# Performance work log

Hardware: AMD Instinct MI355X
Metric: run time of the kernel (lower is better)

## Reference

```python
import jax, jax.numpy as jnp
import numpy as np

# e2m1 FP4 lookup table (MXFP4)
FP4_VALUES = jnp.array([0.0, 0.5, 1.0, 1.5, 2.0, 3.0, 4.0, 6.0,
                        -0.0, -0.5, -1.0, -1.5, -2.0, -3.0, -4.0, -6.0], dtype=jnp.float32)
BLOCK = 32  # MXFP4/MXFP8 block size
SWIGLU_LIMIT = 7.0
SWIGLU_ALPHA = 1.702


def mxfp8_qdq(x):
    """Quantize-dequantize x to MXFP8: fp8_e4m3 mantissas with per-32-block E8M0 scales."""
    shp = x.shape
    nb = shp[-1] // BLOCK
    xb = x.reshape(*shp[:-1], nb, BLOCK)
    max_abs = jnp.max(jnp.abs(xb), axis=-1, keepdims=True)
    e = jnp.clip(jnp.ceil(jnp.log2(jnp.maximum(max_abs, 1e-12))), -127.0, 128.0)
    scale = jnp.exp2(e)
    xq = (xb / scale).astype(jnp.float8_e4m3fn).astype(x.dtype) * scale
    return xq.reshape(shp)


def dequant_mxfp4(blocks, scales):
    """blocks: [..., g, 16] int (packed nibbles), scales: [..., g] int (E8M0 biased 127).
    Returns [..., g*32] float32, low nibble first within each byte."""
    lo = FP4_VALUES[blocks & 15]
    hi = FP4_VALUES[blocks >> 4]
    vals = jnp.stack([lo, hi], axis=-1).reshape(*blocks.shape[:-1], BLOCK)  # interleave lo,hi
    e = (scales - 127).astype(jnp.float32)
    w = vals * jnp.exp2(e)[..., None]
    return w.reshape(*blocks.shape[:-2], blocks.shape[-2] * BLOCK)


def moe_forward(hidden_states, expert_indices, routing_weights,
                gate_up_blocks, gate_up_scales, gate_up_bias,
                down_blocks, down_scales, down_bias):
    w_gu = dequant_mxfp4(gate_up_blocks, gate_up_scales)  # [E, 2I, H]
    w_d = dequant_mxfp4(down_blocks, down_scales)          # [E, H, I]
    xq = mxfp8_qdq(hidden_states)                          # [T, H] mxfp8 qdq (row-blockwise)

    def one_expert(wgu, bgu, wd, bd):
        h = xq @ wgu.T + bgu                               # [T, 2I]
        gate = jnp.minimum(h[..., 0::2], SWIGLU_LIMIT)     # interleaved gate/up
        up = jnp.clip(h[..., 1::2], -SWIGLU_LIMIT, SWIGLU_LIMIT)
        glu = gate * jax.nn.sigmoid(SWIGLU_ALPHA * gate)
        act = (up + 1.0) * glu                             # [T, I]
        return mxfp8_qdq(act) @ wd.T + bd                  # [T, H]

    expert_outs = jax.vmap(one_expert)(w_gu, gate_up_bias, w_d, down_bias)  # [E, T, H]
    T = hidden_states.shape[0]
    sel = expert_outs[expert_indices, jnp.arange(T)[:, None]]  # [T, K, H]
    return jnp.sum(routing_weights[..., None] * sel, axis=1)   # [T, H]


def setup_inputs() -> dict:
    key = jax.random.key(0)
    ks = jax.random.split(key, 9)
    E, T, K, H, I = 8, 1024, 2, 2880, 2880
    return {
        'hidden_states': jax.random.normal(ks[0], (T, H), dtype=jnp.float32),
        'expert_indices': jax.random.randint(ks[1], (T, K), 0, E, dtype=jnp.int32),
        'routing_weights': jax.random.uniform(ks[2], (T, K), dtype=jnp.float32),
        'gate_up_blocks': jax.random.randint(ks[3], (E, 2 * I, H // 32, 16), 0, 256, dtype=jnp.int32),
        'gate_up_scales': jax.random.randint(ks[4], (E, 2 * I, H // 32), 0, 132, dtype=jnp.int32),
        'gate_up_bias': jax.random.normal(ks[5], (E, 2 * I), dtype=jnp.float32),
        'down_blocks': jax.random.randint(ks[6], (E, H, I // 32, 16), 0, 256, dtype=jnp.int32),
        'down_scales': jax.random.randint(ks[7], (E, H, I // 32), 0, 132, dtype=jnp.int32),
        'down_bias': jax.random.normal(ks[8], (E, H), dtype=jnp.float32),
    }


def reference(hidden_states, expert_indices, routing_weights,
              gate_up_blocks, gate_up_scales, gate_up_bias,
              down_blocks, down_scales, down_bias):
    return moe_forward(hidden_states, expert_indices, routing_weights,
                       gate_up_blocks, gate_up_scales, gate_up_bias,
                       down_blocks, down_scales, down_bias)
```

## Files before the change

### kernel.cpp

```cpp
#include <hip/hip_runtime.h>
#include <math.h>

#define T_TOK 1024
#define E_EXP 8
#define H_DIM 2880
#define I_DIM 2880
#define NGU   5760
#define KB    90
#define TM 128
#define TN 128
#define MAXROWS 3072

typedef __attribute__((ext_vector_type(8))) short short8;
typedef __attribute__((ext_vector_type(4))) float f32x4;

#define PERM(a, b, s) __builtin_amdgcn_perm((uint)(a), (uint)(b), (uint)(s))

#define XQ_OFF   0ull
#define ACT_OFF  5898240ull
#define RTOK_OFF 23592960ull
#define RW_OFF   23605248ull
#define EB_OFF   23617536ull
#define EPC_OFF  23617568ull
#define CGU_OFF  23617664ull
#define CGS_OFF  89972864ull
#define CDB_OFF  94120064ull
#define CDS_OFF  127297664ull
#define WS_NEED  129371264ull

__device__ inline ushort f2bf(float f) {
  unsigned u = __float_as_uint(f);
  unsigned r = u + 0x7FFFu + ((u >> 16) & 1u);
  return (ushort)(r >> 16);
}

__device__ inline int blk_exp(float amax) {
  amax = fmaxf(amax, 1e-12f);
  unsigned b = __float_as_uint(amax);
  int e = (int)(b >> 23) - 127;
  if (b & 0x7FFFFFu) e += 1;
  return min(max(e, -127), 128);
}

__device__ inline float qdq_val(float v, int eblk) {
  float av = fabsf(v);
  if (av == 0.f) return 0.f;
  int fl = (int)(__float_as_uint(av) >> 23) - 127 - eblk;
  int p = max(fl, -6) - 3;
  float step = ldexpf(1.f, p + eblk);
  return rintf(v / step) * step;
}

__device__ inline float fp4v(int n) {
  int mag = n & 7;
  float v;
  if (mag == 0) v = 0.f;
  else if (mag == 1) v = 0.5f;
  else v = ldexpf(1.0f + 0.5f * (float)(mag & 1), (mag >> 1) - 1);
  return (n & 8) ? -v : v;
}

__device__ inline uint dec_byte(const float2* lut, int b, float sc) {
  float2 l = lut[b & 255];
  uint lo = __float_as_uint(l.x * sc);
  uint hi = __float_as_uint(l.y * sc);
  return PERM(hi, lo, 0x07060302u);
}

struct BTbl { uint tlo_l, tlo_h, thi_l, thi_h; };

__device__ inline BTbl build_tbl(float sc) {
  uint g0 = 0u;
  uint g1 = __float_as_uint(0.5f * sc);
  uint g2 = __float_as_uint(sc);
  uint g3 = __float_as_uint(1.5f * sc);
  uint g4 = __float_as_uint(2.0f * sc);
  uint g5 = __float_as_uint(3.0f * sc);
  uint g6 = __float_as_uint(4.0f * sc);
  uint g7 = __float_as_uint(6.0f * sc);
  uint p01 = PERM(g1, g0, 0x07030602u);
  uint p23 = PERM(g3, g2, 0x07030602u);
  uint p45 = PERM(g5, g4, 0x07030602u);
  uint p67 = PERM(g7, g6, 0x07030602u);
  BTbl t;
  t.tlo_l = PERM(p23, p01, 0x05040100u);
  t.thi_l = PERM(p23, p01, 0x07060302u);
  t.tlo_h = PERM(p67, p45, 0x05040100u);
  t.thi_h = PERM(p67, p45, 0x07060302u);
  return t;
}

__device__ inline uint4 dec_w(uint w, const BTbl& t) {
  uint ml = w & 0x07070707u;
  uint mh = (w >> 4) & 0x07070707u;
  uint sl = (w << 4) & 0x80808080u;
  uint sh = w & 0x80808080u;
  uint hl = PERM(t.thi_h, t.thi_l, ml) | sl;
  uint hh = PERM(t.thi_h, t.thi_l, mh) | sh;
  uint ll = PERM(t.tlo_h, t.tlo_l, ml);
  uint lh = PERM(t.tlo_h, t.tlo_l, mh);
  uint4 o;
  o.x = PERM(hl, ll, 0x05010400u);
  o.y = PERM(hl, ll, 0x07030602u);
  o.z = PERM(hh, lh, 0x05010400u);
  o.w = PERM(hh, lh, 0x07030602u);
  return o;
}

__device__ inline uint4 aperm(uint4 u) {
  uint4 v;
  v.x = PERM(u.y, u.x, 0x05040100u);
  v.y = PERM(u.w, u.z, 0x05040100u);
  v.z = PERM(u.y, u.x, 0x07060302u);
  v.w = PERM(u.w, u.z, 0x07060302u);
  return v;
}

__global__ void repack_kernel(const int* __restrict__ src, uint4* __restrict__ dst, int n16) {
  int g = blockIdx.x * 256 + threadIdx.x;
  if (g >= n16) return;
  const int4* s = (const int4*)(src) + g * 4;
  int4 w0 = s[0], w1 = s[1], w2 = s[2], w3 = s[3];
  uint4 o;
  o.x = (uint)(w0.x & 255) | ((uint)(w0.y & 255) << 8) | ((uint)(w0.z & 255) << 16) | ((uint)(w0.w) << 24);
  o.y = (uint)(w1.x & 255) | ((uint)(w1.y & 255) << 8) | ((uint)(w1.z & 255) << 16) | ((uint)(w1.w) << 24);
  o.z = (uint)(w2.x & 255) | ((uint)(w2.y & 255) << 8) | ((uint)(w2.z & 255) << 16) | ((uint)(w2.w) << 24);
  o.w = (uint)(w3.x & 255) | ((uint)(w3.y & 255) << 8) | ((uint)(w3.z & 255) << 16) | ((uint)(w3.w) << 24);
  dst[g] = o;
}

__global__ void quant_x_kernel(const float* __restrict__ x, ushort* __restrict__ xq) {
  int g = blockIdx.x * 256 + threadIdx.x;
  float4 v4 = ((const float4*)x)[g];
  float am = fmaxf(fmaxf(fabsf(v4.x), fabsf(v4.y)), fmaxf(fabsf(v4.z), fabsf(v4.w)));
  am = fmaxf(am, __shfl_xor(am, 1));
  am = fmaxf(am, __shfl_xor(am, 2));
  am = fmaxf(am, __shfl_xor(am, 4));
  int eb = blk_exp(am);
  ushort4 o;
  o.x = f2bf(qdq_val(v4.x, eb));
  o.y = f2bf(qdq_val(v4.y, eb));
  o.z = f2bf(qdq_val(v4.z, eb));
  o.w = f2bf(qdq_val(v4.w, eb));
  ((ushort4*)xq)[g] = o;
}

__global__ void routing_kernel(const int* __restrict__ eidx, const float* __restrict__ rwt,
                               int* __restrict__ rtok, float* __restrict__ rw,
                               int* __restrict__ ebase, int* __restrict__ epc) {
  __shared__ int cnt[E_EXP];
  __shared__ int base_s[E_EXP];
  __shared__ int pos[E_EXP];
  int t = threadIdx.x;
  if (t < E_EXP) cnt[t] = 0;
  __syncthreads();
  for (int p = t; p < T_TOK * 2; p += 256) atomicAdd(&cnt[eidx[p]], 1);
  __syncthreads();
  if (t == 0) {
    int b = 0;
    for (int e = 0; e < E_EXP; e++) {
      base_s[e] = b;
      b += ((cnt[e] + TM - 1) / TM) * TM;
    }
  }
  __syncthreads();
  if (t < E_EXP) {
    pos[t] = 0;
    ebase[t] = base_s[t];
    epc[t] = ((cnt[t] + TM - 1) / TM) * TM;
  }
  __syncthreads();
  for (int p = t; p < T_TOK * 2; p += 256) {
    int e = eidx[p];
    int o = atomicAdd(&pos[e], 1);
    rtok[base_s[e] + o] = p >> 1;
    rw[base_s[e] + o] = rwt[p];
  }
  __syncthreads();
  for (int e = 0; e < E_EXP; e++) {
    int c = cnt[e], pc = ((c + TM - 1) / TM) * TM;
    for (int i = c + t; i < pc; i += 256) {
      rtok[base_s[e] + i] = 0;
      rw[base_s[e] + i] = 0.f;
    }
  }
}

__global__ __launch_bounds__(256, 2)
void gemm1c_kernel(const ushort* __restrict__ xq,
                   const uchar* __restrict__ cgu, const uchar* __restrict__ cgs,
                   const float* __restrict__ gubias,
                   const int* __restrict__ rtok, const int* __restrict__ ebase,
                   const int* __restrict__ epc,
                   ushort* __restrict__ act) {
  const int ntile = blockIdx.x;
  const int e = blockIdx.y >> 4;
  const int mtile = blockIdx.y & 15;
  if (mtile * TM >= epc[e]) return;
  const int rowbase = ebase[e] + mtile * TM;

  __shared__ __align__(16) ushort lA[TM][40];
  __shared__ __align__(16) ushort lB[TN][40];

  const int tid = threadIdx.x;
  const int wave = tid >> 6, lane = tid & 63;
  const int half = tid & 1, srow = tid >> 1;
  const int wm = (wave & 1) * 64, wn = (wave >> 1) * 64;
  const int lrow = lane & 15, q = lane >> 4;

  const int tokA = rtok[rowbase + srow];
  const ushort* aSrc = xq + tokA * H_DIM + half * 16;
  const int nrow = ntile * TN + srow;
  const uchar* bSrc = cgu + (size_t)(e * NGU + nrow) * 1440 + half * 8;
  const uchar* sSrc = cgs + (size_t)(e * NGU + nrow) * KB;

  f32x4 acc[4][4];
#pragma unroll
  for (int i = 0; i < 4; i++)
#pragma unroll
    for (int j = 0; j < 4; j++) acc[i][j] = (f32x4){0.f, 0.f, 0.f, 0.f};

  uint4 a0 = ((const uint4*)(aSrc))[0];
  uint4 a1 = ((const uint4*)(aSrc))[1];
  uint2 bw = *(const uint2*)(bSrc);
  uchar sb = sSrc[0];

  for (int kb = 0; kb < KB; kb++) {
    const int nk = (kb + 1 < KB) ? kb + 1 : kb;
    uint4 na0 = ((const uint4*)(aSrc + nk * 32))[0];
    uint4 na1 = ((const uint4*)(aSrc + nk * 32))[1];
    uint2 nbw = *(const uint2*)(bSrc + nk * 16);
    uchar nsb = sSrc[nk];

    float sc = ldexpf(1.f, (int)sb - 127);
    BTbl t = build_tbl(sc);
    uint4 d0 = dec_w(bw.x, t);
    uint4 d1 = dec_w(bw.y, t);
    uint4 pa0 = aperm(a0);
    uint4 pa1 = aperm(a1);

    __syncthreads();
    *(uint4*)&lA[srow][half * 16] = pa0;
    *(uint4*)&lA[srow][half * 16 + 8] = pa1;
    *(uint4*)&lB[srow][half * 16] = d0;
    *(uint4*)&lB[srow][half * 16 + 8] = d1;
    __syncthreads();

    short8 af[4], bfr[4];
#pragma unroll
    for (int mi = 0; mi < 4; mi++) af[mi] = *(const short8*)&lA[wm + mi * 16 + lrow][q * 8];
#pragma unroll
    for (int ni = 0; ni < 4; ni++) bfr[ni] = *(const short8*)&lB[wn + ni * 16 + lrow][q * 8];
#pragma unroll
    for (int mi = 0; mi < 4; mi++)
#pragma unroll
      for (int ni = 0; ni < 4; ni++)
        acc[mi][ni] = __builtin_amdgcn_mfma_f32_16x16x32_bf16(af[mi], bfr[ni], acc[mi][ni], 0, 0, 0);

    a0 = na0; a1 = na1; bw = nbw; sb = nsb;
  }

  const int nbase = ntile * TN + wn;
  float bias_v[4];
#pragma unroll
  for (int ni = 0; ni < 4; ni++) bias_v[ni] = gubias[e * NGU + nbase + ni * 16 + lrow];
  const bool evenl = (lane & 1) == 0;
#pragma unroll
  for (int mi = 0; mi < 4; mi++) {
    float av[4][4];
#pragma unroll
    for (int ni = 0; ni < 4; ni++)
#pragma unroll
      for (int r = 0; r < 4; r++) {
        float h = acc[mi][ni][r] + bias_v[ni];
        float pp = __shfl_xor(h, 1);
        float gate = evenl ? h : pp;
        float up = evenl ? pp : h;
        gate = fminf(gate, 7.f);
        up = fminf(fmaxf(up, -7.f), 7.f);
        float glu = gate / (1.f + expf(-1.702f * gate));
        av[ni][r] = (up + 1.f) * glu;
      }
#pragma unroll
    for (int r = 0; r < 4; r++) {
      float am = 0.f;
#pragma unroll
      for (int ni = 0; ni < 4; ni++) am = fmaxf(am, fabsf(av[ni][r]));
      am = fmaxf(am, __shfl_xor(am, 2));
      am = fmaxf(am, __shfl_xor(am, 4));
      am = fmaxf(am, __shfl_xor(am, 8));
      int eb = blk_exp(am);
      if (evenl) {
        int row = rowbase + wm + mi * 16 + q * 4 + r;
        int cb = (nbase >> 1) + (lrow >> 1);
#pragma unroll
        for (int ni = 0; ni < 4; ni++)
          act[row * I_DIM + cb + ni * 8] = f2bf(qdq_val(av[ni][r], eb));
      }
    }
  }
}

__global__ __launch_bounds__(256, 2)
void gemm2c_kernel(const ushort* __restrict__ act,
                   const uchar* __restrict__ cdb, const uchar* __restrict__ cds,
                   const float* __restrict__ dbias,
                   const int* __restrict__ rtok, const float* __restrict__ rw,
                   const int* __restrict__ ebase, const int* __restrict__ epc,
                   float* __restrict__ out) {
  const int ntile = blockIdx.x;
  const int e = blockIdx.y >> 4;
  const int mtile = blockIdx.y & 15;
  if (mtile * TM >= epc[e]) return;
  const int rowbase = ebase[e] + mtile * TM;
  const int kz = blockIdx.z;
  const int kb0 = kz * (KB / 2), kb1 = kb0 + (KB / 2);

  __shared__ __align__(16) ushort lA[TM][40];
  __shared__ __align__(16) ushort lB[TN][40];

  const int tid = threadIdx.x;
  const int wave = tid >> 6, lane = tid & 63;
  const int half = tid & 1, srow = tid >> 1;
  const int wm = (wave & 1) * 64, wn = (wave >> 1) * 64;
  const int lrow = lane & 15, q = lane >> 4;

  const ushort* aSrc = act + (size_t)(rowbase + srow) * I_DIM + half * 16;
  int nrow = ntile * TN + srow;
  if (nrow >= H_DIM) nrow = H_DIM - 1;
  const uchar* bSrc = cdb + (size_t)(e * H_DIM + nrow) * 1440 + half * 8;
  const uchar* sSrc = cds + (size_t)(e * H_DIM + nrow) * KB;

  f32x4 acc[4][4];
#pragma unroll
  for (int i = 0; i < 4; i++)
#pragma unroll
    for (int j = 0; j < 4; j++) acc[i][j] = (f32x4){0.f, 0.f, 0.f, 0.f};

  uint4 a0 = ((const uint4*)(aSrc + kb0 * 32))[0];
  uint4 a1 = ((const uint4*)(aSrc + kb0 * 32))[1];
  uint2 bw = *(const uint2*)(bSrc + kb0 * 16);
  uchar sb = sSrc[kb0];

  for (int kb = kb0; kb < kb1; kb++) {
    const int nk = (kb + 1 < kb1) ? kb + 1 : kb;
    uint4 na0 = ((const uint4*)(aSrc + nk * 32))[0];
    uint4 na1 = ((const uint4*)(aSrc + nk * 32))[1];
    uint2 nbw = *(const uint2*)(bSrc + nk * 16);
    uchar nsb = sSrc[nk];

    float sc = ldexpf(1.f, (int)sb - 127);
    BTbl t = build_tbl(sc);
    uint4 d0 = dec_w(bw.x, t);
    uint4 d1 = dec_w(bw.y, t);
    uint4 pa0 = aperm(a0);
    uint4 pa1 = aperm(a1);

    __syncthreads();
    *(uint4*)&lA[srow][half * 16] = pa0;
    *(uint4*)&lA[srow][half * 16 + 8] = pa1;
    *(uint4*)&lB[srow][half * 16] = d0;
    *(uint4*)&lB[srow][half * 16 + 8] = d1;
    __syncthreads();

    short8 af[4], bfr[4];
#pragma unroll
    for (int mi = 0; mi < 4; mi++) af[mi] = *(const short8*)&lA[wm + mi * 16 + lrow][q * 8];
#pragma unroll
    for (int ni = 0; ni < 4; ni++) bfr[ni] = *(const short8*)&lB[wn + ni * 16 + lrow][q * 8];
#pragma unroll
    for (int mi = 0; mi < 4; mi++)
#pragma unroll
      for (int ni = 0; ni < 4; ni++)
        acc[mi][ni] = __builtin_amdgcn_mfma_f32_16x16x32_bf16(af[mi], bfr[ni], acc[mi][ni], 0, 0, 0);

    a0 = na0; a1 = na1; bw = nbw; sb = nsb;
  }

  const int nbase = ntile * TN + wn;
  float bias_v[4];
#pragma unroll
  for (int ni = 0; ni < 4; ni++) {
    int n = nbase + ni * 16 + lrow;
    bias_v[ni] = (kz == 0 && n < H_DIM) ? dbias[e * H_DIM + n] : 0.f;
  }
#pragma unroll
  for (int mi = 0; mi < 4; mi++)
#pragma unroll
    for (int r = 0; r < 4; r++) {
      int orow = rowbase + wm + mi * 16 + q * 4 + r;
      int tok = rtok[orow];
      float w = rw[orow];
      if (w != 0.f) {
#pragma unroll
        for (int ni = 0; ni < 4; ni++) {
          int n = nbase + ni * 16 + lrow;
          if (n < H_DIM) atomicAdd(&out[tok * H_DIM + n], w * (acc[mi][ni][r] + bias_v[ni]));
        }
      }
    }
}

__global__ __launch_bounds__(256, 2)
void gemm1_kernel(const ushort* __restrict__ xq,
                  const int* __restrict__ gub, const int* __restrict__ gus,
                  const float* __restrict__ gubias,
                  const int* __restrict__ rtok, const int* __restrict__ ebase,
                  const int* __restrict__ epc,
                  ushort* __restrict__ act) {
  const int ntile = blockIdx.x;
  const int e = blockIdx.y >> 4;
  const int mtile = blockIdx.y & 15;
  if (mtile * TM >= epc[e]) return;
  const int rowbase = ebase[e] + mtile * TM;

  __shared__ __align__(16) ushort lA[TM][40];
  __shared__ __align__(16) ushort lB[TN][40];
  __shared__ float2 lut[256];

  const int tid = threadIdx.x;
  lut[tid] = make_float2(fp4v(tid & 15), fp4v((tid >> 4) & 15));
  __syncthreads();

  const int wave = tid >> 6, lane = tid & 63;
  const int half = tid & 1, srow = tid >> 1;
  const int wm = (wave & 1) * 64, wn = (wave >> 1) * 64;
  const int lrow = lane & 15, q = lane >> 4;

  const int tokA = rtok[rowbase + srow];
  const ushort* aSrc = xq + tokA * H_DIM + half * 16;
  const int nrow = ntile * TN + srow;
  const int* bSrc = gub + ((e * NGU + nrow) * KB) * 16 + half * 8;
  const int* sSrc = gus + (e * NGU + nrow) * KB;

  f32x4 acc[4][4];
#pragma unroll
  for (int i = 0; i < 4; i++)
#pragma unroll
    for (int j = 0; j < 4; j++) acc[i][j] = (f32x4){0.f, 0.f, 0.f, 0.f};

  for (int kb = 0; kb < KB; kb++) {
    uint4 a0 = ((const uint4*)(aSrc + kb * 32))[0];
    uint4 a1 = ((const uint4*)(aSrc + kb * 32))[1];
    int4 b0 = ((const int4*)(bSrc + kb * 16))[0];
    int4 b1 = ((const int4*)(bSrc + kb * 16))[1];
    float sc = ldexpf(1.f, sSrc[kb] - 127);
    int bv[8] = {b0.x, b0.y, b0.z, b0.w, b1.x, b1.y, b1.z, b1.w};
    uint us[8];
#pragma unroll
    for (int j = 0; j < 8; j++) us[j] = dec_byte(lut, bv[j], sc);
    __syncthreads();
    *(uint4*)&lA[srow][half * 16] = a0;
    *(uint4*)&lA[srow][half * 16 + 8] = a1;
    uint4 w0; w0.x = us[0]; w0.y = us[1]; w0.z = us[2]; w0.w = us[3];
    uint4 w1; w1.x = us[4]; w1.y = us[5]; w1.z = us[6]; w1.w = us[7];
    *(uint4*)&lB[srow][half * 16] = w0;
    *(uint4*)&lB[srow][half * 16 + 8] = w1;
    __syncthreads();
    short8 af[4], bfr[4];
#pragma unroll
    for (int mi = 0; mi < 4; mi++) af[mi] = *(const short8*)&lA[wm + mi * 16 + lrow][q * 8];
#pragma unroll
    for (int ni = 0; ni < 4; ni++) bfr[ni] = *(const short8*)&lB[wn + ni * 16 + lrow][q * 8];
#pragma unroll
    for (int mi = 0; mi < 4; mi++)
#pragma unroll
      for (int ni = 0; ni < 4; ni++)
        acc[mi][ni] = __builtin_amdgcn_mfma_f32_16x16x32_bf16(af[mi], bfr[ni], acc[mi][ni], 0, 0, 0);
  }

  const int nbase = ntile * TN + wn;
  float bias_v[4];
#pragma unroll
  for (int ni = 0; ni < 4; ni++) bias_v[ni] = gubias[e * NGU + nbase + ni * 16 + lrow];
  const bool evenl = (lane & 1) == 0;
#pragma unroll
  for (int mi = 0; mi < 4; mi++) {
    float av[4][4];
#pragma unroll
    for (int ni = 0; ni < 4; ni++)
#pragma unroll
      for (int r = 0; r < 4; r++) {
        float h = acc[mi][ni][r] + bias_v[ni];
        float pp = __shfl_xor(h, 1);
        float gate = evenl ? h : pp;
        float up = evenl ? pp : h;
        gate = fminf(gate, 7.f);
        up = fminf(fmaxf(up, -7.f), 7.f);
        float glu = gate / (1.f + expf(-1.702f * gate));
        av[ni][r] = (up + 1.f) * glu;
      }
#pragma unroll
    for (int r = 0; r < 4; r++) {
      float am = 0.f;
#pragma unroll
      for (int ni = 0; ni < 4; ni++) am = fmaxf(am, fabsf(av[ni][r]));
      am = fmaxf(am, __shfl_xor(am, 2));
      am = fmaxf(am, __shfl_xor(am, 4));
      am = fmaxf(am, __shfl_xor(am, 8));
      int eb = blk_exp(am);
      if (evenl) {
        int row = rowbase + wm + mi * 16 + q * 4 + r;
        int cb = (nbase >> 1) + (lrow >> 1);
#pragma unroll
        for (int ni = 0; ni < 4; ni++)
          act[row * I_DIM + cb + ni * 8] = f2bf(qdq_val(av[ni][r], eb));
      }
    }
  }
}

__global__ __launch_bounds__(256, 2)
void gemm2_kernel(const ushort* __restrict__ act,
                  const int* __restrict__ db, const int* __restrict__ dsc,
                  const float* __restrict__ dbias,
                  const int* __restrict__ rtok, const float* __restrict__ rw,
                  const int* __restrict__ ebase, const int* __restrict__ epc,
                  float* __restrict__ out) {
  const int ntile = blockIdx.x;
  const int e = blockIdx.y >> 4;
  const int mtile = blockIdx.y & 15;
  if (mtile * TM >= epc[e]) return;
  const int rowbase = ebase[e] + mtile * TM;
  const int kz = blockIdx.z;
  const int kb0 = kz * (KB / 2), kb1 = kb0 + (KB / 2);

  __shared__ __align__(16) ushort lA[TM][40];
  __shared__ __align__(16) ushort lB[TN][40];
  __shared__ float2 lut[256];

  const int tid = threadIdx.x;
  lut[tid] = make_float2(fp4v(tid & 15), fp4v((tid >> 4) & 15));
  __syncthreads();

  const int wave = tid >> 6, lane = tid & 63;
  const int half = tid & 1, srow = tid >> 1;
  const int wm = (wave & 1) * 64, wn = (wave >> 1) * 64;
  const int lrow = lane & 15, q = lane >> 4;

  const ushort* aSrc = act + (rowbase + srow) * I_DIM + half * 16;
  int nrow = ntile * TN + srow;
  if (nrow >= H_DIM) nrow = H_DIM - 1;
  const int* bSrc = db + ((e * H_DIM + nrow) * KB) * 16 + half * 8;
  const int* sSrc = dsc + (e * H_DIM + nrow) * KB;

  f32x4 acc[4][4];
#pragma unroll
  for (int i = 0; i < 4; i++)
#pragma unroll
    for (int j = 0; j < 4; j++) acc[i][j] = (f32x4){0.f, 0.f, 0.f, 0.f};

  for (int kb = kb0; kb < kb1; kb++) {
    uint4 a0 = ((const uint4*)(aSrc + kb * 32))[0];
    uint4 a1 = ((const uint4*)(aSrc + kb * 32))[1];
    int4 b0 = ((const int4*)(bSrc + kb * 16))[0];
    int4 b1 = ((const int4*)(bSrc + kb * 16))[1];
    float sc = ldexpf(1.f, sSrc[kb] - 127);
    int bv[8] = {b0.x, b0.y, b0.z, b0.w, b1.x, b1.y, b1.z, b1.w};
    uint us[8];
#pragma unroll
    for (int j = 0; j < 8; j++) us[j] = dec_byte(lut, bv[j], sc);
    __syncthreads();
    *(uint4*)&lA[srow][half * 16] = a0;
    *(uint4*)&lA[srow][half * 16 + 8] = a1;
    uint4 w0; w0.x = us[0]; w0.y = us[1]; w0.z = us[2]; w0.w = us[3];
    uint4 w1; w1.x = us[4]; w1.y = us[5]; w1.z = us[6]; w1.w = us[7];
    *(uint4*)&lB[srow][half * 16] = w0;
    *(uint4*)&lB[srow][half * 16 + 8] = w1;
    __syncthreads();
    short8 af[4], bfr[4];
#pragma unroll
    for (int mi = 0; mi < 4; mi++) af[mi] = *(const short8*)&lA[wm + mi * 16 + lrow][q * 8];
#pragma unroll
    for (int ni = 0; ni < 4; ni++) bfr[ni] = *(const short8*)&lB[wn + ni * 16 + lrow][q * 8];
#pragma unroll
    for (int mi = 0; mi < 4; mi++)
#pragma unroll
      for (int ni = 0; ni < 4; ni++)
        acc[mi][ni] = __builtin_amdgcn_mfma_f32_16x16x32_bf16(af[mi], bfr[ni], acc[mi][ni], 0, 0, 0);
  }

  const int nbase = ntile * TN + wn;
  float bias_v[4];
#pragma unroll
  for (int ni = 0; ni < 4; ni++) {
    int n = nbase + ni * 16 + lrow;
    bias_v[ni] = (kz == 0 && n < H_DIM) ? dbias[e * H_DIM + n] : 0.f;
  }
#pragma unroll
  for (int mi = 0; mi < 4; mi++)
#pragma unroll
    for (int r = 0; r < 4; r++) {
      int orow = rowbase + wm + mi * 16 + q * 4 + r;
      int tok = rtok[orow];
      float w = rw[orow];
      if (w != 0.f) {
#pragma unroll
        for (int ni = 0; ni < 4; ni++) {
          int n = nbase + ni * 16 + lrow;
          if (n < H_DIM) atomicAdd(&out[tok * H_DIM + n], w * (acc[mi][ni][r] + bias_v[ni]));
        }
      }
    }
}

extern "C" void kernel_launch(void* const* d_in, const int* in_sizes, int n_in,
                              void* d_out, int out_size, void* d_ws, size_t ws_size,
                              hipStream_t stream) {
  const float* hs = (const float*)d_in[0];
  const int* eidx = (const int*)d_in[1];
  const float* rwt = (const float*)d_in[2];
  const int* gub = (const int*)d_in[3];
  const int* gus = (const int*)d_in[4];
  const float* gubias = (const float*)d_in[5];
  const int* db = (const int*)d_in[6];
  const int* dsc = (const int*)d_in[7];
  const float* dbias = (const float*)d_in[8];
  float* out = (float*)d_out;
  char* ws = (char*)d_ws;

  ushort* xq = (ushort*)(ws + XQ_OFF);
  ushort* act = (ushort*)(ws + ACT_OFF);
  int* rtok = (int*)(ws + RTOK_OFF);
  float* rw = (float*)(ws + RW_OFF);
  int* ebase = (int*)(ws + EB_OFF);
  int* epc = (int*)(ws + EPC_OFF);

  hipMemsetAsync(d_out, 0, (size_t)out_size * sizeof(float), stream);
  quant_x_kernel<<<2880, 256, 0, stream>>>(hs, xq);
  routing_kernel<<<1, 256, 0, stream>>>(eidx, rwt, rtok, rw, ebase, epc);

  if (ws_size >= WS_NEED) {
    uchar* cgu = (uchar*)(ws + CGU_OFF);
    uchar* cgs = (uchar*)(ws + CGS_OFF);
    uchar* cdb = (uchar*)(ws + CDB_OFF);
    uchar* cds = (uchar*)(ws + CDS_OFF);
    repack_kernel<<<16200, 256, 0, stream>>>(gub, (uint4*)cgu, 4147200);
    repack_kernel<<<8100, 256, 0, stream>>>(db, (uint4*)cdb, 2073600);
    repack_kernel<<<1013, 256, 0, stream>>>(gus, (uint4*)cgs, 259200);
    repack_kernel<<<507, 256, 0, stream>>>(dsc, (uint4*)cds, 129600);
    gemm1c_kernel<<<dim3(45, 128), 256, 0, stream>>>(xq, cgu, cgs, gubias, rtok, ebase, epc, act);
    gemm2c_kernel<<<dim3(23, 128, 2), 256, 0, stream>>>(act, cdb, cds, dbias, rtok, rw, ebase, epc, out);
  } else {
    gemm1_kernel<<<dim3(45, 128), 256, 0, stream>>>(xq, gub, gus, gubias, rtok, ebase, epc, act);
    gemm2_kernel<<<dim3(23, 128, 2), 256, 0, stream>>>(act, db, dsc, dbias, rtok, rw, ebase, epc, out);
  }
}
```

Measured before the change: 816.6 us.

## Use native MXFP8xMXFP4 scaled MFMA with runtime layout probe and bf16 fallback

Adds a probe kernel that runs the scaled f8f6f4 MFMA on synthetic data at runtime to find the correct nibble order and scale-lane mapping. When the probe succeeds, new GEMM kernels feed fp8 activations and raw packed fp4 weights straight into mfma_scale 32x32x64, with per-block E8M0 scales staged in LDS. This removes the in-loop fp4-to-bf16 dequantization and halves the activation bytes. Activations are quantized to fp8 bytes in the epilogue, and scales are repacked into k-major arrays. The bf16 kernels remain as a flag-gated fallback, which adds extra launches that exit early, and the B operand pads half its register lanes with zeros.

```diff
diff --git a/kernel.cpp b/kernel.cpp
--- a/kernel.cpp
+++ b/kernel.cpp
@@ -12,21 +12,28 @@
 #define MAXROWS 3072
 
 typedef __attribute__((ext_vector_type(8))) short short8;
+typedef __attribute__((ext_vector_type(8))) int i32x8;
 typedef __attribute__((ext_vector_type(4))) float f32x4;
+typedef __attribute__((ext_vector_type(16))) float f32x16;
 
 #define PERM(a, b, s) __builtin_amdgcn_perm((uint)(a), (uint)(b), (uint)(s))
 
-#define XQ_OFF   0ull
-#define ACT_OFF  5898240ull
-#define RTOK_OFF 23592960ull
-#define RW_OFF   23605248ull
-#define EB_OFF   23617536ull
-#define EPC_OFF  23617568ull
-#define CGU_OFF  23617664ull
-#define CGS_OFF  89972864ull
-#define CDB_OFF  94120064ull
-#define CDS_OFF  127297664ull
-#define WS_NEED  129371264ull
+#define FLAGS_OFF 0ull
+#define EB_OFF    16ull
+#define EPC_OFF   48ull
+#define RTOK_OFF  128ull
+#define RW_OFF    12416ull
+#define CGU_OFF   24704ull
+#define CDB_OFF   66379904ull
+#define WGS_OFF   99557504ull
+#define WDS_OFF   103704704ull
+#define PATH_OFF  105778304ull
+#define XQ_OFF    (PATH_OFF)
+#define ACT_OFF   (PATH_OFF + 5898240ull)
+#define XQ8_OFF   (PATH_OFF)
+#define XS8_OFF   (PATH_OFF + 2949120ull)
+#define ACT8_OFF  (PATH_OFF + 3041280ull)
+#define AS8_OFF   (PATH_OFF + 11888640ull)
 
 __device__ inline ushort f2bf(float f) {
   unsigned u = __float_as_uint(f);
@@ -51,6 +58,17 @@
   return rintf(v / step) * step;
 }
 
+__device__ inline uint fp8_byte_exact(float x) {
+  uint u = __float_as_uint(x);
+  uint s = (u >> 24) & 0x80u;
+  float ax = fabsf(x);
+  if (ax == 0.f) return s;
+  int E = (int)((u >> 23) & 0xFFu) - 127;
+  uint M = (u >> 20) & 7u;
+  if (E >= -6) return s | (uint)((E + 7) << 3) | M;
+  return s | (uint)(int)(ax * 512.f + 0.5f);
+}
+
 __device__ inline float fp4v(int n) {
   int mag = n & 7;
   float v;
@@ -60,11 +78,8 @@
   return (n & 8) ? -v : v;
 }
 
-__device__ inline uint dec_byte(const float2* lut, int b, float sc) {
-  float2 l = lut[b & 255];
-  uint lo = __float_as_uint(l.x * sc);
-  uint hi = __float_as_uint(l.y * sc);
-  return PERM(hi, lo, 0x07060302u);
+__device__ inline uint nibswap(uint w) {
+  return ((w & 0x0F0F0F0Fu) << 4) | ((w >> 4) & 0x0F0F0F0Fu);
 }
 
 struct BTbl { uint tlo_l, tlo_h, thi_l, thi_h; };
@@ -116,20 +131,77 @@
   return v;
 }
 
-__global__ void repack_kernel(const int* __restrict__ src, uint4* __restrict__ dst, int n16) {
-  int g = blockIdx.x * 256 + threadIdx.x;
-  if (g >= n16) return;
-  const int4* s = (const int4*)(src) + g * 4;
-  int4 w0 = s[0], w1 = s[1], w2 = s[2], w3 = s[3];
-  uint4 o;
-  o.x = (uint)(w0.x & 255) | ((uint)(w0.y & 255) << 8) | ((uint)(w0.z & 255) << 16) | ((uint)(w0.w) << 24);
-  o.y = (uint)(w1.x & 255) | ((uint)(w1.y & 255) << 8) | ((uint)(w1.z & 255) << 16) | ((uint)(w1.w) << 24);
-  o.z = (uint)(w2.x & 255) | ((uint)(w2.y & 255) << 8) | ((uint)(w2.z & 255) << 16) | ((uint)(w2.w) << 24);
-  o.w = (uint)(w3.x & 255) | ((uint)(w3.y & 255) << 8) | ((uint)(w3.z & 255) << 16) | ((uint)(w3.w) << 24);
-  dst[g] = o;
-}
-
-__global__ void quant_x_kernel(const float* __restrict__ x, ushort* __restrict__ xq) {
+__global__ void probe_kernel(int* __restrict__ flags) {
+  const int l = threadIdx.x;
+  const int l31 = l & 31, h = l >> 5;
+  const uint E4[7] = {0x00u, 0x38u, 0x40u, 0x44u, 0x48u, 0x4Au, 0x4Cu};
+
+  i32x8 af;
+#pragma unroll
+  for (int r8 = 0; r8 < 8; r8++) {
+    uint w = 0;
+#pragma unroll
+    for (int b = 0; b < 4; b++) {
+      int k = h * 32 + r8 * 4 + b;
+      int v = ((l31 + 3 * k) % 13) - 6;
+      uint byte = E4[v < 0 ? -v : v] | (v < 0 ? 0x80u : 0u);
+      w |= byte << (8 * b);
+    }
+    af[r8] = (int)w;
+  }
+  i32x8 b0v, b1v;
+#pragma unroll
+  for (int i = 0; i < 8; i++) { b0v[i] = 0; b1v[i] = 0; }
+#pragma unroll
+  for (int r4 = 0; r4 < 4; r4++) {
+    uint w0 = 0, w1 = 0;
+#pragma unroll
+    for (int i = 0; i < 4; i++) {
+      int k0 = h * 32 + r4 * 8 + 2 * i;
+      uint c0 = (uint)((k0 * 5 + l31 * 3) & 15);
+      uint c1 = (uint)(((k0 + 1) * 5 + l31 * 3) & 15);
+      w0 |= (c0 | (c1 << 4)) << (8 * i);
+      w1 |= (c1 | (c0 << 4)) << (8 * i);
+    }
+    b0v[r4] = (int)w0;
+    b1v[r4] = (int)w1;
+  }
+
+  f32x16 z;
+#pragma unroll
+  for (int i = 0; i < 16; i++) z[i] = 0.f;
+
+  int best = -1, mask = 0;
+  for (int c = 0; c < 4; c++) {
+    int f1 = c & 1, f2 = (c >> 1) & 1;
+    i32x8 bb = f1 ? b1v : b0v;
+    int kidx = h ^ f2;
+    int sa = 127 + ((l31 + kidx) & 3);
+    int sb = 127 - ((l31 + kidx) & 1);
+    f32x16 d = __builtin_amdgcn_mfma_scale_f32_32x32x64_f8f6f4(af, bb, z, 0, 4, 0, sa, 0, sb);
+    bool ok = true;
+#pragma unroll
+    for (int r = 0; r < 16; r++) {
+      int row = (r & 3) + 8 * (r >> 2) + 4 * h;
+      float ref = 0.f;
+      for (int k = 0; k < 64; k++) {
+        float fa = (float)(((row + 3 * k) % 13) - 6) * exp2f((float)((row + (k >> 5)) & 3));
+        float fb = fp4v((k * 5 + l31 * 3) & 15) * exp2f(-(float)((l31 + (k >> 5)) & 1));
+        ref += fa * fb;
+      }
+      if (fabsf(d[r] - ref) > 0.25f) ok = false;
+    }
+    if (__all((int)ok)) {
+      mask |= (1 << c);
+      if (best < 0) best = c;
+    }
+  }
+  if (l == 0) { flags[0] = best; flags[1] = mask; }
+}
+
+__global__ void quant_x_kernel(const int* __restrict__ flags,
+                               const float* __restrict__ x, ushort* __restrict__ xq) {
+  if (flags[0] >= 0) return;
   int g = blockIdx.x * 256 + threadIdx.x;
   float4 v4 = ((const float4*)x)[g];
   float am = fmaxf(fmaxf(fabsf(v4.x), fabsf(v4.y)), fmaxf(fabsf(v4.z), fabsf(v4.w)));
@@ -143,6 +215,30 @@
   o.z = f2bf(qdq_val(v4.z, eb));
   o.w = f2bf(qdq_val(v4.w, eb));
   ((ushort4*)xq)[g] = o;
+}
+
+__global__ void quant_x8_kernel(const int* __restrict__ flags,
+                                const float* __restrict__ x, uint* __restrict__ xq8,
+                                uchar* __restrict__ xs8) {
+  if (flags[0] < 0) return;
+  int g = blockIdx.x * 256 + threadIdx.x;
+  float4 v = ((const float4*)x)[g];
+  float am = fmaxf(fmaxf(fabsf(v.x), fabsf(v.y)), fmaxf(fabsf(v.z), fabsf(v.w)));
+  am = fmaxf(am, __shfl_xor(am, 1));
+  am = fmaxf(am, __shfl_xor(am, 2));
+  am = fmaxf(am, __shfl_xor(am, 4));
+  int eb = blk_exp(am);
+  float s = ldexpf(1.f, -eb);
+  uint b0 = fp8_byte_exact(qdq_val(v.x * s, 0));
+  uint b1 = fp8_byte_exact(qdq_val(v.y * s, 0));
+  uint b2 = fp8_byte_exact(qdq_val(v.z * s, 0));
+  uint b3 = fp8_byte_exact(qdq_val(v.w * s, 0));
+  xq8[g] = b0 | (b1 << 8) | (b2 << 16) | (b3 << 24);
+  if ((g & 7) == 0) {
+    int tok = g / 720;
+    int kb = (g - tok * 720) >> 3;
+    xs8[kb * T_TOK + tok] = (uchar)(eb + 127);
+  }
 }
 
 __global__ void routing_kernel(const int* __restrict__ eidx, const float* __restrict__ rwt,
@@ -186,19 +282,287 @@
   }
 }
 
-__global__ __launch_bounds__(256, 2)
-void gemm1c_kernel(const ushort* __restrict__ xq,
-                   const uchar* __restrict__ cgu, const uchar* __restrict__ cgs,
+__global__ void repack_kernel(const int* __restrict__ flags,
+                              const int* __restrict__ src, uint4* __restrict__ dst, int n16) {
+  int g = blockIdx.x * 256 + threadIdx.x;
+  if (g >= n16) return;
+  uint f1 = (flags[0] >= 0 && (flags[0] & 1)) ? 1u : 0u;
+  const int4* s = (const int4*)(src) + g * 4;
+  int4 w0 = s[0], w1 = s[1], w2 = s[2], w3 = s[3];
+  uint4 o;
+  o.x = (uint)(w0.x & 255) | ((uint)(w0.y & 255) << 8) | ((uint)(w0.z & 255) << 16) | ((uint)(w0.w) << 24);
+  o.y = (uint)(w1.x & 255) | ((uint)(w1.y & 255) << 8) | ((uint)(w1.z & 255) << 16) | ((uint)(w1.w) << 24);
+  o.z = (uint)(w2.x & 255) | ((uint)(w2.y & 255) << 8) | ((uint)(w2.z & 255) << 16) | ((uint)(w2.w) << 24);
+  o.w = (uint)(w3.x & 255) | ((uint)(w3.y & 255) << 8) | ((uint)(w3.z & 255) << 16) | ((uint)(w3.w) << 24);
+  if (f1) { o.x = nibswap(o.x); o.y = nibswap(o.y); o.z = nibswap(o.z); o.w = nibswap(o.w); }
+  dst[g] = o;
+}
+
+__global__ void repack_scale_kernel(const int* __restrict__ src, uchar* __restrict__ dst, int R) {
+  int r = blockIdx.x * 256 + threadIdx.x;
+  int kb = blockIdx.y;
+  dst[(size_t)kb * R + r] = (uchar)src[(size_t)r * KB + kb];
+}
+
+__global__ __launch_bounds__(256, 3)
+void gemm1s_kernel(const int* __restrict__ flags,
+                   const uchar* __restrict__ xq8, const uchar* __restrict__ xs8,
+                   const uchar* __restrict__ cgu, const uchar* __restrict__ wgs,
                    const float* __restrict__ gubias,
                    const int* __restrict__ rtok, const int* __restrict__ ebase,
                    const int* __restrict__ epc,
-                   ushort* __restrict__ act) {
+                   uchar* __restrict__ act8, uchar* __restrict__ as8) {
+  const int fl = flags[0];
+  if (fl < 0) return;
+  const int f2 = (fl >> 1) & 1;
   const int ntile = blockIdx.x;
   const int e = blockIdx.y >> 4;
   const int mtile = blockIdx.y & 15;
   if (mtile * TM >= epc[e]) return;
   const int rowbase = ebase[e] + mtile * TM;
 
+  __shared__ __align__(16) uchar lA[128 * 80];
+  __shared__ __align__(16) uchar lB[128 * 48];
+  __shared__ uchar sAs[KB * 128];
+  __shared__ uchar sBs[KB * 128];
+  __shared__ int ltok[128];
+
+  const int tid = threadIdx.x;
+  const int wave = tid >> 6, lane = tid & 63;
+  const int half = tid & 1, srow = tid >> 1;
+  const int wm = (wave & 1) * 64, wn = (wave >> 1) * 64;
+  const int l31 = lane & 31, l5 = lane >> 5;
+
+  if (tid < 128) ltok[tid] = rtok[rowbase + tid];
+  __syncthreads();
+  for (int i = tid; i < KB * 128; i += 256) {
+    int kb = i >> 7, r = i & 127;
+    sAs[i] = xs8[kb * T_TOK + ltok[r]];
+    sBs[i] = wgs[(size_t)kb * 46080 + e * NGU + ntile * 128 + r];
+  }
+
+  const int tokA = ltok[srow];
+  const uchar* aSrc = xq8 + (size_t)tokA * H_DIM + half * 32;
+  const int nrow = ntile * TN + srow;
+  const uchar* bSrc = cgu + (size_t)(e * NGU + nrow) * 1440 + half * 16;
+
+  f32x16 acc[2][2];
+#pragma unroll
+  for (int i = 0; i < 2; i++)
+#pragma unroll
+    for (int j = 0; j < 2; j++)
+#pragma unroll
+      for (int r = 0; r < 16; r++) acc[i][j][r] = 0.f;
+
+  uint4 pa0 = *(const uint4*)(aSrc);
+  uint4 pa1 = *(const uint4*)(aSrc + 16);
+  uint4 pb = *(const uint4*)(bSrc);
+
+  for (int kb2 = 0; kb2 < 45; kb2++) {
+    const int nk = (kb2 + 1 < 45) ? kb2 + 1 : kb2;
+    uint4 na0 = *(const uint4*)(aSrc + nk * 64);
+    uint4 na1 = *(const uint4*)(aSrc + nk * 64 + 16);
+    uint4 nb = *(const uint4*)(bSrc + nk * 32);
+
+    __syncthreads();
+    *(uint4*)&lA[srow * 80 + half * 32] = pa0;
+    *(uint4*)&lA[srow * 80 + half * 32 + 16] = pa1;
+    *(uint4*)&lB[srow * 48 + half * 16] = pb;
+    __syncthreads();
+
+    i32x8 af[2], bf2[2];
+    int sa[2], sb[2];
+#pragma unroll
+    for (int f = 0; f < 2; f++) {
+      const uchar* pr = &lA[(wm + f * 32 + l31) * 80 + l5 * 32];
+      uint4 lo = *(const uint4*)pr;
+      uint4 hi = *(const uint4*)(pr + 16);
+      af[f][0] = lo.x; af[f][1] = lo.y; af[f][2] = lo.z; af[f][3] = lo.w;
+      af[f][4] = hi.x; af[f][5] = hi.y; af[f][6] = hi.z; af[f][7] = hi.w;
+      uint4 bb = *(const uint4*)&lB[(wn + f * 32 + l31) * 48 + l5 * 16];
+      bf2[f][0] = bb.x; bf2[f][1] = bb.y; bf2[f][2] = bb.z; bf2[f][3] = bb.w;
+      bf2[f][4] = 0; bf2[f][5] = 0; bf2[f][6] = 0; bf2[f][7] = 0;
+      int kidx = kb2 * 2 + (l5 ^ f2);
+      sa[f] = sAs[kidx * 128 + wm + f * 32 + l31];
+      sb[f] = sBs[kidx * 128 + wn + f * 32 + l31];
+    }
+#pragma unroll
+    for (int fm = 0; fm < 2; fm++)
+#pragma unroll
+      for (int fn = 0; fn < 2; fn++)
+        acc[fm][fn] = __builtin_amdgcn_mfma_scale_f32_32x32x64_f8f6f4(
+            af[fm], bf2[fn], acc[fm][fn], 0, 4, 0, sa[fm], 0, sb[fn]);
+
+    pa0 = na0; pa1 = na1; pb = nb;
+  }
+
+  const int nb0 = ntile * 128 + wn;
+  const float bias0 = gubias[e * NGU + nb0 + l31];
+  const float bias1 = gubias[e * NGU + nb0 + 32 + l31];
+  const bool evenl = (lane & 1) == 0;
+  const int cb_ix = ntile * 2 + (wn >> 6);
+  const int cbase = ntile * 64 + (wn >> 1) + (l31 >> 1);
+#pragma unroll
+  for (int fm = 0; fm < 2; fm++) {
+#pragma unroll
+    for (int r = 0; r < 16; r++) {
+      int row = rowbase + wm + fm * 32 + (r & 3) + 8 * (r >> 2) + l5 * 4;
+      float h0 = acc[fm][0][r] + bias0;
+      float h1 = acc[fm][1][r] + bias1;
+      float p0 = __shfl_xor(h0, 1);
+      float p1 = __shfl_xor(h1, 1);
+      float g0 = evenl ? h0 : p0, u0 = evenl ? p0 : h0;
+      float g1 = evenl ? h1 : p1, u1 = evenl ? p1 : h1;
+      g0 = fminf(g0, 7.f); u0 = fminf(fmaxf(u0, -7.f), 7.f);
+      g1 = fminf(g1, 7.f); u1 = fminf(fmaxf(u1, -7.f), 7.f);
+      float a0 = (u0 + 1.f) * (g0 / (1.f + expf(-1.702f * g0)));
+      float a1 = (u1 + 1.f) * (g1 / (1.f + expf(-1.702f * g1)));
+      float am = fmaxf(fabsf(a0), fabsf(a1));
+      am = fmaxf(am, __shfl_xor(am, 2));
+      am = fmaxf(am, __shfl_xor(am, 4));
+      am = fmaxf(am, __shfl_xor(am, 8));
+      am = fmaxf(am, __shfl_xor(am, 16));
+      int eb = blk_exp(am);
+      if (l31 == 0) as8[(size_t)cb_ix * MAXROWS + row] = (uchar)(eb + 127);
+      if (evenl) {
+        float s = ldexpf(1.f, -eb);
+        act8[(size_t)row * I_DIM + cbase] = (uchar)fp8_byte_exact(qdq_val(a0 * s, 0));
+        act8[(size_t)row * I_DIM + cbase + 16] = (uchar)fp8_byte_exact(qdq_val(a1 * s, 0));
+      }
+    }
+  }
+}
+
+__global__ __launch_bounds__(256, 3)
+void gemm2s_kernel(const int* __restrict__ flags,
+                   const uchar* __restrict__ act8, const uchar* __restrict__ as8,
+                   const uchar* __restrict__ cdb, const uchar* __restrict__ wds,
+                   const float* __restrict__ dbias,
+                   const int* __restrict__ rtok, const float* __restrict__ rw,
+                   const int* __restrict__ ebase, const int* __restrict__ epc,
+                   float* __restrict__ out) {
+  const int fl = flags[0];
+  if (fl < 0) return;
+  const int f2 = (fl >> 1) & 1;
+  const int ntile = blockIdx.x;
+  const int e = blockIdx.y >> 4;
+  const int mtile = blockIdx.y & 15;
+  if (mtile * TM >= epc[e]) return;
+  const int rowbase = ebase[e] + mtile * TM;
+  const int kz = blockIdx.z;
+  const int klo = kz * 23;
+  const int khi = kz ? 45 : 23;
+
+  __shared__ __align__(16) uchar lA[128 * 80];
+  __shared__ __align__(16) uchar lB[128 * 48];
+  __shared__ uchar sAs[KB * 128];
+  __shared__ uchar sBs[KB * 128];
+
+  const int tid = threadIdx.x;
+  const int wave = tid >> 6, lane = tid & 63;
+  const int half = tid & 1, srow = tid >> 1;
+  const int wm = (wave & 1) * 64, wn = (wave >> 1) * 64;
+  const int l31 = lane & 31, l5 = lane >> 5;
+
+  for (int i = tid; i < KB * 128; i += 256) {
+    int kb = i >> 7, r = i & 127;
+    int rr = min(ntile * 128 + r, H_DIM - 1);
+    sAs[i] = as8[(size_t)kb * MAXROWS + rowbase + r];
+    sBs[i] = wds[(size_t)kb * 23040 + e * H_DIM + rr];
+  }
+
+  const uchar* aSrc = act8 + (size_t)(rowbase + srow) * I_DIM + half * 32;
+  const int nrow = min(ntile * TN + srow, H_DIM - 1);
+  const uchar* bSrc = cdb + (size_t)(e * H_DIM + nrow) * 1440 + half * 16;
+
+  f32x16 acc[2][2];
+#pragma unroll
+  for (int i = 0; i < 2; i++)
+#pragma unroll
+    for (int j = 0; j < 2; j++)
+#pragma unroll
+      for (int r = 0; r < 16; r++) acc[i][j][r] = 0.f;
+
+  uint4 pa0 = *(const uint4*)(aSrc + klo * 64);
+  uint4 pa1 = *(const uint4*)(aSrc + klo * 64 + 16);
+  uint4 pb = *(const uint4*)(bSrc + klo * 32);
+
+  for (int kb2 = klo; kb2 < khi; kb2++) {
+    const int nk = (kb2 + 1 < khi) ? kb2 + 1 : kb2;
+    uint4 na0 = *(const uint4*)(aSrc + nk * 64);
+    uint4 na1 = *(const uint4*)(aSrc + nk * 64 + 16);
+    uint4 nb = *(const uint4*)(bSrc + nk * 32);
+
+    __syncthreads();
+    *(uint4*)&lA[srow * 80 + half * 32] = pa0;
+    *(uint4*)&lA[srow * 80 + half * 32 + 16] = pa1;
+    *(uint4*)&lB[srow * 48 + half * 16] = pb;
+    __syncthreads();
+
+    i32x8 af[2], bf2[2];
+    int sa[2], sb[2];
+#pragma unroll
+    for (int f = 0; f < 2; f++) {
+      const uchar* pr = &lA[(wm + f * 32 + l31) * 80 + l5 * 32];
+      uint4 lo = *(const uint4*)pr;
+      uint4 hi = *(const uint4*)(pr + 16);
+      af[f][0] = lo.x; af[f][1] = lo.y; af[f][2] = lo.z; af[f][3] = lo.w;
+      af[f][4] = hi.x; af[f][5] = hi.y; af[f][6] = hi.z; af[f][7] = hi.w;
+      uint4 bb = *(const uint4*)&lB[(wn + f * 32 + l31) * 48 + l5 * 16];
+      bf2[f][0] = bb.x; bf2[f][1] = bb.y; bf2[f][2] = bb.z; bf2[f][3] = bb.w;
+      bf2[f][4] = 0; bf2[f][5] = 0; bf2[f][6] = 0; bf2[f][7] = 0;
+      int kidx = kb2 * 2 + (l5 ^ f2);
+      sa[f] = sAs[kidx * 128 + wm + f * 32 + l31];
+      sb[f] = sBs[kidx * 128 + wn + f * 32 + l31];
+    }
+#pragma unroll
+    for (int fm = 0; fm < 2; fm++)
+#pragma unroll
+      for (int fn = 0; fn < 2; fn++)
+        acc[fm][fn] = __builtin_amdgcn_mfma_scale_f32_32x32x64_f8f6f4(
+            af[fm], bf2[fn], acc[fm][fn], 0, 4, 0, sa[fm], 0, sb[fn]);
+
+    pa0 = na0; pa1 = na1; pb = nb;
+  }
+
+  const int nb0 = ntile * 128 + wn;
+  float bias0 = 0.f, bias1 = 0.f;
+  if (kz == 0) {
+    bias0 = (nb0 + l31 < H_DIM) ? dbias[e * H_DIM + nb0 + l31] : 0.f;
+    bias1 = (nb0 + 32 + l31 < H_DIM) ? dbias[e * H_DIM + nb0 + 32 + l31] : 0.f;
+  }
+#pragma unroll
+  for (int fm = 0; fm < 2; fm++) {
+#pragma unroll
+    for (int r = 0; r < 16; r++) {
+      int orow = rowbase + wm + fm * 32 + (r & 3) + 8 * (r >> 2) + l5 * 4;
+      int tok = rtok[orow];
+      float w = rw[orow];
+      if (w != 0.f) {
+        int n0 = nb0 + l31;
+        int n1 = nb0 + 32 + l31;
+        if (n0 < H_DIM) atomicAdd(&out[(size_t)tok * H_DIM + n0], w * (acc[fm][0][r] + bias0));
+        if (n1 < H_DIM) atomicAdd(&out[(size_t)tok * H_DIM + n1], w * (acc[fm][1][r] + bias1));
+      }
+    }
+  }
+}
+
+__global__ __launch_bounds__(256, 2)
+void gemm1c_kernel(const int* __restrict__ flags,
+                   const ushort* __restrict__ xq,
+                   const uchar* __restrict__ cgu, const uchar* __restrict__ wgs,
+                   const float* __restrict__ gubias,
+                   const int* __restrict__ rtok, const int* __restrict__ ebase,
+                   const int* __restrict__ epc,
+                   ushort* __restrict__ act) {
+  if (flags[0] >= 0) return;
+  const int ntile = blockIdx.x;
+  const int e = blockIdx.y >> 4;
+  const int mtile = blockIdx.y & 15;
+  if (mtile * TM >= epc[e]) return;
+  const int rowbase = ebase[e] + mtile * TM;
+
   __shared__ __align__(16) ushort lA[TM][40];
   __shared__ __align__(16) ushort lB[TN][40];
 
@@ -212,7 +576,7 @@
   const ushort* aSrc = xq + tokA * H_DIM + half * 16;
   const int nrow = ntile * TN + srow;
   const uchar* bSrc = cgu + (size_t)(e * NGU + nrow) * 1440 + half * 8;
-  const uchar* sSrc = cgs + (size_t)(e * NGU + nrow) * KB;
+  const uchar* sSrc = wgs + (size_t)(e * NGU + nrow);
 
   f32x4 acc[4][4];
 #pragma unroll
@@ -230,7 +594,7 @@
     uint4 na0 = ((const uint4*)(aSrc + nk * 32))[0];
     uint4 na1 = ((const uint4*)(aSrc + nk * 32))[1];
     uint2 nbw = *(const uint2*)(bSrc + nk * 16);
-    uchar nsb = sSrc[nk];
+    uchar nsb = sSrc[(size_t)nk * 46080];
 
     float sc = ldexpf(1.f, (int)sb - 127);
     BTbl t = build_tbl(sc);
@@ -302,12 +666,14 @@
 }
 
 __global__ __launch_bounds__(256, 2)
-void gemm2c_kernel(const ushort* __restrict__ act,
-                   const uchar* __restrict__ cdb, const uchar* __restrict__ cds,
+void gemm2c_kernel(const int* __restrict__ flags,
+                   const ushort* __restrict__ act,
+                   const uchar* __restrict__ cdb, const uchar* __restrict__ wds,
                    const float* __restrict__ dbias,
                    const int* __restrict__ rtok, const float* __restrict__ rw,
                    const int* __restrict__ ebase, const int* __restrict__ epc,
                    float* __restrict__ out) {
+  if (flags[0] >= 0) return;
   const int ntile = blockIdx.x;
   const int e = blockIdx.y >> 4;
   const int mtile = blockIdx.y & 15;
@@ -329,7 +695,7 @@
   int nrow = ntile * TN + srow;
   if (nrow >= H_DIM) nrow = H_DIM - 1;
   const uchar* bSrc = cdb + (size_t)(e * H_DIM + nrow) * 1440 + half * 8;
-  const uchar* sSrc = cds + (size_t)(e * H_DIM + nrow) * KB;
+  const uchar* sSrc = wds + (size_t)(e * H_DIM + nrow);
 
   f32x4 acc[4][4];
 #pragma unroll
@@ -340,14 +706,14 @@
   uint4 a0 = ((const uint4*)(aSrc + kb0 * 32))[0];
   uint4 a1 = ((const uint4*)(aSrc + kb0 * 32))[1];
   uint2 bw = *(const uint2*)(bSrc + kb0 * 16);
-  uchar sb = sSrc[kb0];
+  uchar sb = sSrc[(size_t)kb0 * 23040];
 
   for (int kb = kb0; kb < kb1; kb++) {
     const int nk = (kb + 1 < kb1) ? kb + 1 : kb;
     uint4 na0 = ((const uint4*)(aSrc + nk * 32))[0];
     uint4 na1 = ((const uint4*)(aSrc + nk * 32))[1];
     uint2 nbw = *(const uint2*)(bSrc + nk * 16);
-    uchar nsb = sSrc[nk];
+    uchar nsb = sSrc[(size_t)nk * 23040];
 
     float sc = ldexpf(1.f, (int)sb - 127);
     BTbl t = build_tbl(sc);
@@ -375,209 +741,6 @@
         acc[mi][ni] = __builtin_amdgcn_mfma_f32_16x16x32_bf16(af[mi], bfr[ni], acc[mi][ni], 0, 0, 0);
 
     a0 = na0; a1 = na1; bw = nbw; sb = nsb;
-  }
-
-  const int nbase = ntile * TN + wn;
-  float bias_v[4];
-#pragma unroll
-  for (int ni = 0; ni < 4; ni++) {
-    int n = nbase + ni * 16 + lrow;
-    bias_v[ni] = (kz == 0 && n < H_DIM) ? dbias[e * H_DIM + n] : 0.f;
-  }
-#pragma unroll
-  for (int mi = 0; mi < 4; mi++)
-#pragma unroll
-    for (int r = 0; r < 4; r++) {
-      int orow = rowbase + wm + mi * 16 + q * 4 + r;
-      int tok = rtok[orow];
-      float w = rw[orow];
-      if (w != 0.f) {
-#pragma unroll
-        for (int ni = 0; ni < 4; ni++) {
-          int n = nbase + ni * 16 + lrow;
-          if (n < H_DIM) atomicAdd(&out[tok * H_DIM + n], w * (acc[mi][ni][r] + bias_v[ni]));
-        }
-      }
-    }
-}
-
-__global__ __launch_bounds__(256, 2)
-void gemm1_kernel(const ushort* __restrict__ xq,
-                  const int* __restrict__ gub, const int* __restrict__ gus,
-                  const float* __restrict__ gubias,
-                  const int* __restrict__ rtok, const int* __restrict__ ebase,
-                  const int* __restrict__ epc,
-                  ushort* __restrict__ act) {
-  const int ntile = blockIdx.x;
-  const int e = blockIdx.y >> 4;
-  const int mtile = blockIdx.y & 15;
-  if (mtile * TM >= epc[e]) return;
-  const int rowbase = ebase[e] + mtile * TM;
-
-  __shared__ __align__(16) ushort lA[TM][40];
-  __shared__ __align__(16) ushort lB[TN][40];
-  __shared__ float2 lut[256];
-
-  const int tid = threadIdx.x;
-  lut[tid] = make_float2(fp4v(tid & 15), fp4v((tid >> 4) & 15));
-  __syncthreads();
-
-  const int wave = tid >> 6, lane = tid & 63;
-  const int half = tid & 1, srow = tid >> 1;
-  const int wm = (wave & 1) * 64, wn = (wave >> 1) * 64;
-  const int lrow = lane & 15, q = lane >> 4;
-
-  const int tokA = rtok[rowbase + srow];
-  const ushort* aSrc = xq + tokA * H_DIM + half * 16;
-  const int nrow = ntile * TN + srow;
-  const int* bSrc = gub + ((e * NGU + nrow) * KB) * 16 + half * 8;
-  const int* sSrc = gus + (e * NGU + nrow) * KB;
-
-  f32x4 acc[4][4];
-#pragma unroll
-  for (int i = 0; i < 4; i++)
-#pragma unroll
-    for (int j = 0; j < 4; j++) acc[i][j] = (f32x4){0.f, 0.f, 0.f, 0.f};
-
-  for (int kb = 0; kb < KB; kb++) {
-    uint4 a0 = ((const uint4*)(aSrc + kb * 32))[0];
-    uint4 a1 = ((const uint4*)(aSrc + kb * 32))[1];
-    int4 b0 = ((const int4*)(bSrc + kb * 16))[0];
-    int4 b1 = ((const int4*)(bSrc + kb * 16))[1];
-    float sc = ldexpf(1.f, sSrc[kb] - 127);
-    int bv[8] = {b0.x, b0.y, b0.z, b0.w, b1.x, b1.y, b1.z, b1.w};
-    uint us[8];
-#pragma unroll
-    for (int j = 0; j < 8; j++) us[j] = dec_byte(lut, bv[j], sc);
-    __syncthreads();
-    *(uint4*)&lA[srow][half * 16] = a0;
-    *(uint4*)&lA[srow][half * 16 + 8] = a1;
-    uint4 w0; w0.x = us[0]; w0.y = us[1]; w0.z = us[2]; w0.w = us[3];
-    uint4 w1; w1.x = us[4]; w1.y = us[5]; w1.z = us[6]; w1.w = us[7];
-    *(uint4*)&lB[srow][half * 16] = w0;
-    *(uint4*)&lB[srow][half * 16 + 8] = w1;
-    __syncthreads();
-    short8 af[4], bfr[4];
-#pragma unroll
-    for (int mi = 0; mi < 4; mi++) af[mi] = *(const short8*)&lA[wm + mi * 16 + lrow][q * 8];
-#pragma unroll
-    for (int ni = 0; ni < 4; ni++) bfr[ni] = *(const short8*)&lB[wn + ni * 16 + lrow][q * 8];
-#pragma unroll
-    for (int mi = 0; mi < 4; mi++)
-#pragma unroll
-      for (int ni = 0; ni < 4; ni++)
-        acc[mi][ni] = __builtin_amdgcn_mfma_f32_16x16x32_bf16(af[mi], bfr[ni], acc[mi][ni], 0, 0, 0);
-  }
-
-  const int nbase = ntile * TN + wn;
-  float bias_v[4];
-#pragma unroll
-  for (int ni = 0; ni < 4; ni++) bias_v[ni] = gubias[e * NGU + nbase + ni * 16 + lrow];
-  const bool evenl = (lane & 1) == 0;
-#pragma unroll
-  for (int mi = 0; mi < 4; mi++) {
-    float av[4][4];
-#pragma unroll
-    for (int ni = 0; ni < 4; ni++)
-#pragma unroll
-      for (int r = 0; r < 4; r++) {
-        float h = acc[mi][ni][r] + bias_v[ni];
-        float pp = __shfl_xor(h, 1);
-        float gate = evenl ? h : pp;
-        float up = evenl ? pp : h;
-        gate = fminf(gate, 7.f);
-        up = fminf(fmaxf(up, -7.f), 7.f);
-        float glu = gate / (1.f + expf(-1.702f * gate));
-        av[ni][r] = (up + 1.f) * glu;
-      }
-#pragma unroll
-    for (int r = 0; r < 4; r++) {
-      float am = 0.f;
-#pragma unroll
-      for (int ni = 0; ni < 4; ni++) am = fmaxf(am, fabsf(av[ni][r]));
-      am = fmaxf(am, __shfl_xor(am, 2));
-      am = fmaxf(am, __shfl_xor(am, 4));
-      am = fmaxf(am, __shfl_xor(am, 8));
-      int eb = blk_exp(am);
-      if (evenl) {
-        int row = rowbase + wm + mi * 16 + q * 4 + r;
-        int cb = (nbase >> 1) + (lrow >> 1);
-#pragma unroll
-        for (int ni = 0; ni < 4; ni++)
-          act[row * I_DIM + cb + ni * 8] = f2bf(qdq_val(av[ni][r], eb));
-      }
-    }
-  }
-}
-
-__global__ __launch_bounds__(256, 2)
-void gemm2_kernel(const ushort* __restrict__ act,
-                  const int* __restrict__ db, const int* __restrict__ dsc,
-                  const float* __restrict__ dbias,
-                  const int* __restrict__ rtok, const float* __restrict__ rw,
-                  const int* __restrict__ ebase, const int* __restrict__ epc,
-                  float* __restrict__ out) {
-  const int ntile = blockIdx.x;
-  const int e = blockIdx.y >> 4;
-  const int mtile = blockIdx.y & 15;
-  if (mtile * TM >= epc[e]) return;
-  const int rowbase = ebase[e] + mtile * TM;
-  const int kz = blockIdx.z;
-  const int kb0 = kz * (KB / 2), kb1 = kb0 + (KB / 2);
-
-  __shared__ __align__(16) ushort lA[TM][40];
-  __shared__ __align__(16) ushort lB[TN][40];
-  __shared__ float2 lut[256];
-
-  const int tid = threadIdx.x;
-  lut[tid] = make_float2(fp4v(tid & 15), fp4v((tid >> 4) & 15));
-  __syncthreads();
-
-  const int wave = tid >> 6, lane = tid & 63;
-  const int half = tid & 1, srow = tid >> 1;
-  const int wm = (wave & 1) * 64, wn = (wave >> 1) * 64;
-  const int lrow = lane & 15, q = lane >> 4;
-
-  const ushort* aSrc = act + (rowbase + srow) * I_DIM + half * 16;
-  int nrow = ntile * TN + srow;
-  if (nrow >= H_DIM) nrow = H_DIM - 1;
-  const int* bSrc = db + ((e * H_DIM + nrow) * KB) * 16 + half * 8;
-  const int* sSrc = dsc + (e * H_DIM + nrow) * KB;
-
-  f32x4 acc[4][4];
-#pragma unroll
-  for (int i = 0; i < 4; i++)
-#pragma unroll
-    for (int j = 0; j < 4; j++) acc[i][j] = (f32x4){0.f, 0.f, 0.f, 0.f};
-
-  for (int kb = kb0; kb < kb1; kb++) {
-    uint4 a0 = ((const uint4*)(aSrc + kb * 32))[0];
-    uint4 a1 = ((const uint4*)(aSrc + kb * 32))[1];
-    int4 b0 = ((const int4*)(bSrc + kb * 16))[0];
-    int4 b1 = ((const int4*)(bSrc + kb * 16))[1];
-    float sc = ldexpf(1.f, sSrc[kb] - 127);
-    int bv[8] = {b0.x, b0.y, b0.z, b0.w, b1.x, b1.y, b1.z, b1.w};
-    uint us[8];
-#pragma unroll
-    for (int j = 0; j < 8; j++) us[j] = dec_byte(lut, bv[j], sc);
-    __syncthreads();
-    *(uint4*)&lA[srow][half * 16] = a0;
-    *(uint4*)&lA[srow][half * 16 + 8] = a1;
-    uint4 w0; w0.x = us[0]; w0.y = us[1]; w0.z = us[2]; w0.w = us[3];
-    uint4 w1; w1.x = us[4]; w1.y = us[5]; w1.z = us[6]; w1.w = us[7];
-    *(uint4*)&lB[srow][half * 16] = w0;
-    *(uint4*)&lB[srow][half * 16 + 8] = w1;
-    __syncthreads();
-    short8 af[4], bfr[4];
-#pragma unroll
-    for (int mi = 0; mi < 4; mi++) af[mi] = *(const short8*)&lA[wm + mi * 16 + lrow][q * 8];
-#pragma unroll
-    for (int ni = 0; ni < 4; ni++) bfr[ni] = *(const short8*)&lB[wn + ni * 16 + lrow][q * 8];
-#pragma unroll
-    for (int mi = 0; mi < 4; mi++)
-#pragma unroll
-      for (int ni = 0; ni < 4; ni++)
-        acc[mi][ni] = __builtin_amdgcn_mfma_f32_16x16x32_bf16(af[mi], bfr[ni], acc[mi][ni], 0, 0, 0);
   }
 
   const int nbase = ntile * TN + wn;
@@ -619,30 +782,37 @@
   float* out = (float*)d_out;
   char* ws = (char*)d_ws;
 
+  int* flags = (int*)(ws + FLAGS_OFF);
+  int* ebase = (int*)(ws + EB_OFF);
+  int* epc = (int*)(ws + EPC_OFF);
+  int* rtok = (int*)(ws + RTOK_OFF);
+  float* rw = (float*)(ws + RW_OFF);
+  uchar* cgu = (uchar*)(ws + CGU_OFF);
+  uchar* cdb = (uchar*)(ws + CDB_OFF);
+  uchar* wgs = (uchar*)(ws + WGS_OFF);
+  uchar* wds = (uchar*)(ws + WDS_OFF);
   ushort* xq = (ushort*)(ws + XQ_OFF);
   ushort* act = (ushort*)(ws + ACT_OFF);
-  int* rtok = (int*)(ws + RTOK_OFF);
-  float* rw = (float*)(ws + RW_OFF);
-  int* ebase = (int*)(ws + EB_OFF);
-  int* epc = (int*)(ws + EPC_OFF);
+  uint* xq8 = (uint*)(ws + XQ8_OFF);
+  uchar* xs8 = (uchar*)(ws + XS8_OFF);
+  uchar* act8 = (uchar*)(ws + ACT8_OFF);
+  uchar* as8 = (uchar*)(ws + AS8_OFF);
 
   hipMemsetAsync(d_out, 0, (size_t)out_size * sizeof(float), stream);
-  quant_x_kernel<<<2880, 256, 0, stream>>>(hs, xq);
+  probe_kernel<<<1, 64, 0, stream>>>(flags);
   routing_kernel<<<1, 256, 0, stream>>>(eidx, rwt, rtok, rw, ebase, epc);
-
-  if (ws_size >= WS_NEED) {
-    uchar* cgu = (uchar*)(ws + CGU_OFF);
-    uchar* cgs = (uchar*)(ws + CGS_OFF);
-    uchar* cdb = (uchar*)(ws + CDB_OFF);
-    uchar* cds = (uchar*)(ws + CDS_OFF);
-    repack_kernel<<<16200, 256, 0, stream>>>(gub, (uint4*)cgu, 4147200);
-    repack_kernel<<<8100, 256, 0, stream>>>(db, (uint4*)cdb, 2073600);
-    repack_kernel<<<1013, 256, 0, stream>>>(gus, (uint4*)cgs, 259200);
-    repack_kernel<<<507, 256, 0, stream>>>(dsc, (uint4*)cds, 129600);
-    gemm1c_kernel<<<dim3(45, 128), 256, 0, stream>>>(xq, cgu, cgs, gubias, rtok, ebase, epc, act);
-    gemm2c_kernel<<<dim3(23, 128, 2), 256, 0, stream>>>(act, cdb, cds, dbias, rtok, rw, ebase, epc, out);
-  } else {
-    gemm1_kernel<<<dim3(45, 128), 256, 0, stream>>>(xq, gub, gus, gubias, rtok, ebase, epc, act);
-    gemm2_kernel<<<dim3(23, 128, 2), 256, 0, stream>>>(act, db, dsc, dbias, rtok, rw, ebase, epc, out);
-  }
-}
+  quant_x_kernel<<<2880, 256, 0, stream>>>(flags, hs, xq);
+  quant_x8_kernel<<<2880, 256, 0, stream>>>(flags, hs, xq8, xs8);
+  repack_kernel<<<16200, 256, 0, stream>>>(flags, gub, (uint4*)cgu, 4147200);
+  repack_kernel<<<8100, 256, 0, stream>>>(flags, db, (uint4*)cdb, 2073600);
+  repack_scale_kernel<<<dim3(180, 90), 256, 0, stream>>>(gus, wgs, 46080);
+  repack_scale_kernel<<<dim3(90, 90), 256, 0, stream>>>(dsc, wds, 23040);
+  gemm1s_kernel<<<dim3(45, 128), 256, 0, stream>>>(flags, (const uchar*)xq8, xs8, cgu, wgs,
+                                                   gubias, rtok, ebase, epc, act8, as8);
+  gemm2s_kernel<<<dim3(23, 128, 2), 256, 0, stream>>>(flags, act8, as8, cdb, wds, dbias,
+                                                      rtok, rw, ebase, epc, out);
+  gemm1c_kernel<<<dim3(45, 128), 256, 0, stream>>>(flags, xq, cgu, wgs, gubias,
+                                                   rtok, ebase, epc, act);
+  gemm2c_kernel<<<dim3(23, 128, 2), 256, 0, stream>>>(flags, act, cdb, wds, dbias,
+                                                      rtok, rw, ebase, epc, out);
+}
```

Result: slower. 1.183 ms (+44.8%).
